# Kernel tuning notes

Measured on AMD Instinct MI355X. Metric: run time of the kernel, lower is better.

## Reference

```python
import jax, jax.numpy as jnp
import numpy as np

HIDDEN = 1024
NUM_HEADS = 8
HEAD_DIM = HIDDEN // NUM_HEADS
ROPE_BASE = 10000.0
RMS_EPS = 1e-6


def _rotate_half(x):
    # interleaved rotate: (x0,x1,x2,x3,...) -> (-x1,x0,-x3,x2,...)
    x1 = x[..., ::2]
    x2 = x[..., 1::2]
    return jnp.stack([-x2, x1], axis=-1).reshape(x.shape)


def _rope_cos_sin(seq_len, rotary_dim, dtype):
    inv_freq = 1.0 / (ROPE_BASE ** (jnp.arange(0, rotary_dim, 2, dtype=jnp.float32) / rotary_dim))
    pos = jnp.arange(seq_len, dtype=jnp.float32)
    freqs = pos[:, None] * inv_freq[None, :]            # [S, rd/2]
    cos = jnp.repeat(jnp.cos(freqs), 2, axis=-1)        # [S, rd]
    sin = jnp.repeat(jnp.sin(freqs), 2, axis=-1)
    return cos.astype(dtype)[None, None], sin.astype(dtype)[None, None]


def setup_inputs() -> dict:
    key = jax.random.key(0)
    k = jax.random.split(key, 8)
    B, S, H = 2, 2048, HIDDEN
    hidden_states = jax.random.normal(k[0], (B, S, H), dtype=jnp.float32)
    attention_mask = jax.random.randint(k[1], (B, S, S), 0, 2) > 0
    rel_ts_bias = jax.random.normal(k[2], (B, S, S), dtype=jnp.float32)
    s1 = 1.0 / np.sqrt(H)
    W_qkvu = jax.random.normal(k[3], (H, H * 6), dtype=jnp.float32) * s1
    W_out = jax.random.normal(k[4], (H * 3, H), dtype=jnp.float32) * (1.0 / np.sqrt(H * 3))
    b_out = jnp.zeros((H,), dtype=jnp.float32)
    rms_weight = jnp.ones((H,), dtype=jnp.float32)
    return {"hidden_states": hidden_states, "attention_mask": attention_mask,
            "rel_ts_bias": rel_ts_bias, "W_qkvu": W_qkvu, "W_out": W_out,
            "b_out": b_out, "rms_weight": rms_weight}


def reference(hidden_states, attention_mask, rel_ts_bias, W_qkvu, W_out, b_out, rms_weight):
    B, S, H = hidden_states.shape
    nh, hd = NUM_HEADS, HEAD_DIM
    fused = jax.nn.silu(hidden_states @ W_qkvu)          # [B,S,6H]
    gated = fused[..., :3 * H]                            # [B,S,3H]
    v = fused[..., 3 * H:4 * H].reshape(B, S, nh, hd).transpose(0, 2, 1, 3)
    q = fused[..., 4 * H:5 * H].reshape(B, S, nh, hd).transpose(0, 2, 1, 3)
    kk = fused[..., 5 * H:].reshape(B, S, nh, hd).transpose(0, 2, 1, 3)

    cos, sin = _rope_cos_sin(S, hd, hidden_states.dtype)  # rotary_dim == head_dim
    q_rope = q * cos + _rotate_half(q) * sin
    k_rope = kk * cos + _rotate_half(kk) * sin

    inv_s = 1.0 / max(S, 1)
    qk = jax.nn.relu(jnp.einsum('bhnd,bhmd->bhnm', q, kk)) * inv_s
    qk_rope = jax.nn.relu(jnp.einsum('bhnd,bhmd->bhnm', q_rope, k_rope)) * inv_s

    mask = attention_mask[:, None]                        # [B,1,S,S]
    qk = jnp.where(mask, qk, 0.0)
    qk_rope = jnp.where(mask, qk_rope, 0.0)
    ts_bias = jnp.where(attention_mask, rel_ts_bias, 0.0)

    ts_out = jnp.einsum('bnm,bhmd->bnhd', ts_bias, v)
    rope_out = jnp.einsum('bhnm,bhmd->bnhd', qk_rope, v)
    plain_out = jnp.einsum('bhnm,bhmd->bnhd', qk, v)

    combined = jnp.concatenate([rope_out, ts_out, plain_out], axis=-1).reshape(B, S, 3 * H)
    out = (combined * gated) @ W_out + b_out
    y = out + hidden_states
    rms = jax.lax.rsqrt(jnp.mean(y * y, axis=-1, keepdims=True) + RMS_EPS)
    return y * rms * rms_weight
```

## Files before the change

### kernel.cpp

```cpp
#include <hip/hip_runtime.h>
#include <math.h>

static constexpr int Bz = 2;
static constexpr int Sq = 2048;
static constexpr int Hh = 1024;
static constexpr int NH = 8;
static constexpr int HD = 128;
static constexpr int H3 = 3072;
static constexpr int H6 = 6144;

typedef unsigned short ushort_t;
typedef float f32x4v __attribute__((ext_vector_type(4)));
typedef short s16x8 __attribute__((ext_vector_type(8)));

static constexpr size_t FUSED_OFF = 0;
static constexpr size_t A2_OFF    = 12582912;
static constexpr size_t HB_OFF    = 18874368;
static constexpr size_t MTB_OFF   = 18874368;
static constexpr size_t WQT_OFF   = 20971520;
static constexpr size_t WOT_OFF   = 24117248;
static constexpr size_t QR_OFF    = 25690112;
static constexpr size_t KR_OFF    = 27787264;
static constexpr size_t VT_OFF    = 29884416;
static constexpr size_t TAB_OFF   = 31981568;
static constexpr size_t FLAG_OFF  = 32243712;
static constexpr size_t TSB_OFF   = 32243716;

__device__ __forceinline__ float silu_(float x) { return x / (1.0f + expf(-x)); }
__device__ __forceinline__ ushort_t f2bf(float x) {
  unsigned int u = __float_as_uint(x);
  u += 0x7fffu + ((u >> 16) & 1u);
  return (ushort_t)(u >> 16);
}
__device__ __forceinline__ float bf2f(ushort_t u) {
  return __uint_as_float(((unsigned int)u) << 16);
}
__device__ __forceinline__ void g2l16(const ushort_t* g, ushort_t* l) {
  __builtin_amdgcn_global_load_lds(
      (const __attribute__((address_space(1))) unsigned int*)g,
      (__attribute__((address_space(3))) unsigned int*)l, 16, 0, 0);
}

__global__ __launch_bounds__(256) void hstu_pre(const unsigned int* __restrict__ m,
                                                int* __restrict__ flag,
                                                float* __restrict__ tab) {
  __shared__ int s_any;
  if (blockIdx.x == 512) {
    if (threadIdx.x == 0) s_any = 0;
    __syncthreads();
    int any = 0;
    for (int i = threadIdx.x; i < 8192; i += 256)
      if (m[i] > 1u) any = 1;
    if (any) s_any = 1;
    __syncthreads();
    if (threadIdx.x == 0) *flag = s_any;
    return;
  }
  int t = blockIdx.x * 256 + threadIdx.x;
  int i = t & 63;
  int s = t >> 6;
  float inv = powf(10000.0f, -(float)i / 64.0f);
  float sn, cs;
  sincosf((float)s * inv, &sn, &cs);
  tab[2 * t + 0] = cs;
  tab[2 * t + 1] = sn;
}

__global__ __launch_bounds__(256) void hstu_msk(const int* __restrict__ mask32,
                                                const unsigned char* __restrict__ mask8,
                                                const int* __restrict__ mflag,
                                                const float* __restrict__ bias,
                                                ushort_t* __restrict__ tsb,
                                                ushort_t* __restrict__ mtb) {
  const size_t base = ((size_t)blockIdx.x * 256 + threadIdx.x) * 8;
  const int m_u8 = *mflag;
  const ushort_t ivs = f2bf(1.0f / 2048.0f);
  int mk[8];
  if (m_u8) {
    uchar4 a = *(const uchar4*)&mask8[base];
    uchar4 b = *(const uchar4*)&mask8[base + 4];
    mk[0] = a.x; mk[1] = a.y; mk[2] = a.z; mk[3] = a.w;
    mk[4] = b.x; mk[5] = b.y; mk[6] = b.z; mk[7] = b.w;
  } else {
    int4 a = *(const int4*)&mask32[base];
    int4 b = *(const int4*)&mask32[base + 4];
    mk[0] = a.x; mk[1] = a.y; mk[2] = a.z; mk[3] = a.w;
    mk[4] = b.x; mk[5] = b.y; mk[6] = b.z; mk[7] = b.w;
  }
  float4 b0 = *(const float4*)&bias[base];
  float4 b1 = *(const float4*)&bias[base + 4];
  float bb[8] = {b0.x, b0.y, b0.z, b0.w, b1.x, b1.y, b1.z, b1.w};
  ushort_t ts[8], mt[8];
#pragma unroll
  for (int i = 0; i < 8; ++i) {
    ts[i] = f2bf(mk[i] ? bb[i] : 0.0f);
    mt[i] = mk[i] ? ivs : (ushort_t)0u;
  }
  *(s16x8*)&tsb[base] = *(s16x8*)ts;
  *(s16x8*)&mtb[base] = *(s16x8*)mt;
}

__global__ __launch_bounds__(256) void hstu_cvt_all(const float* __restrict__ hidden,
                                                    ushort_t* __restrict__ hb,
                                                    const float* __restrict__ Wq,
                                                    ushort_t* __restrict__ wqt,
                                                    const float* __restrict__ Wo,
                                                    ushort_t* __restrict__ wot) {
  __shared__ float tbuf[32][33];
  const int blk = blockIdx.x;
  if (blk < 4096) {
    const int idx = blk * 256 + threadIdx.x;
    float4 v = *(const float4*)&hidden[(size_t)idx * 4];
    ushort4 o;
    o.x = f2bf(v.x); o.y = f2bf(v.y); o.z = f2bf(v.z); o.w = f2bf(v.w);
    *(ushort4*)&hb[(size_t)idx * 4] = o;
    return;
  }
  const float* in;
  ushort_t* out;
  int K, N, n0, k0;
  if (blk < 4096 + 6144) {
    const int j = blk - 4096;
    in = Wq; out = wqt; K = 1024; N = 6144;
    n0 = (j % 192) * 32; k0 = (j / 192) * 32;
  } else {
    const int j = blk - 10240;
    in = Wo; out = wot; K = 3072; N = 1024;
    n0 = (j % 32) * 32; k0 = (j / 32) * 32;
  }
  const int c = threadIdx.x & 31, rr = threadIdx.x >> 5;
#pragma unroll
  for (int p = 0; p < 4; ++p)
    tbuf[rr + p * 8][c] = in[(size_t)(k0 + rr + p * 8) * N + n0 + c];
  __syncthreads();
#pragma unroll
  for (int p = 0; p < 4; ++p)
    out[(size_t)(n0 + rr + p * 8) * K + k0 + c] = f2bf(tbuf[c][rr + p * 8]);
}

__global__ __launch_bounds__(256) void hstu_prep2(const ushort_t* __restrict__ fused,
                                                  const float2* __restrict__ tab,
                                                  ushort_t* __restrict__ qr,
                                                  ushort_t* __restrict__ kr,
                                                  ushort_t* __restrict__ vt) {
  __shared__ ushort_t tbuf[32][36];
  const int blk = blockIdx.x;
  if (blk < 2048) {
    const int idx = blk * 256 + threadIdx.x;
    const int row = idx >> 7;
    const int cg = (idx & 127) * 8;
    const int s = row & (Sq - 1);
    const float2* trow = &tab[(size_t)s * 64 + ((cg & 127) >> 1)];
    float2 t[4];
#pragma unroll
    for (int p = 0; p < 4; ++p) t[p] = trow[p];
    s16x8 q8 = *(const s16x8*)&fused[(size_t)row * H6 + 4 * Hh + cg];
    s16x8 k8 = *(const s16x8*)&fused[(size_t)row * H6 + 5 * Hh + cg];
    ushort_t qo[8], ko[8];
#pragma unroll
    for (int p = 0; p < 4; ++p) {
      float qx = bf2f((ushort_t)q8[2 * p]), qy = bf2f((ushort_t)q8[2 * p + 1]);
      float kx = bf2f((ushort_t)k8[2 * p]), ky = bf2f((ushort_t)k8[2 * p + 1]);
      qo[2 * p] = f2bf(qx * t[p].x - qy * t[p].y);
      qo[2 * p + 1] = f2bf(qy * t[p].x + qx * t[p].y);
      ko[2 * p] = f2bf(kx * t[p].x - ky * t[p].y);
      ko[2 * p + 1] = f2bf(ky * t[p].x + kx * t[p].y);
    }
    *(s16x8*)&qr[(size_t)row * Hh + cg] = *(s16x8*)qo;
    *(s16x8*)&kr[(size_t)row * Hh + cg] = *(s16x8*)ko;
    return;
  }
  const int j = blk - 2048;
  const int m0 = (j & 63) * 32, d0 = ((j >> 6) & 3) * 32, bh = j >> 8;
  const int b = bh >> 3, h = bh & 7;
  const int r = threadIdx.x >> 3, cg = (threadIdx.x & 7) * 4;
  *(ushort4*)&tbuf[r][cg] =
      *(const ushort4*)&fused[(size_t)(b * Sq + m0 + r) * H6 + 3 * Hh + h * HD + d0 + cg];
  __syncthreads();
  ushort4 o;
  o.x = tbuf[cg + 0][r]; o.y = tbuf[cg + 1][r]; o.z = tbuf[cg + 2][r]; o.w = tbuf[cg + 3][r];
  *(ushort4*)&vt[(size_t)(bh * HD + d0 + r) * Sq + m0 + cg] = o;
}

__global__ __launch_bounds__(256) void hstu_gemm_silu(const ushort_t* __restrict__ A,
                                                      const ushort_t* __restrict__ Bt,
                                                      ushort_t* __restrict__ C) {
  constexpr int K = 1024, N = H6;
  __shared__ ushort_t As[128 * 64];
  __shared__ ushort_t Bs[128 * 64];
  const int tid = threadIdx.x, lane = tid & 63, wid = tid >> 6;
  const int lo4 = lane & 15, hi2 = lane >> 4;
  const int wr = wid >> 1, wc = wid & 1;
  const int row0 = blockIdx.y * 128, col0 = blockIdx.x * 128;
  const int srow = lane >> 3, scol = (lane & 7) * 8;
  f32x4v acc[4][4];
#pragma unroll
  for (int i = 0; i < 4; ++i)
#pragma unroll
    for (int j = 0; j < 4; ++j) acc[i][j] = {0.f, 0.f, 0.f, 0.f};

  for (int k0 = 0; k0 < K; k0 += 64) {
    __syncthreads();
#pragma unroll
    for (int i = 0; i < 4; ++i) {
      const int rb = wid * 32 + i * 8;
      g2l16(&A[(size_t)(row0 + rb + srow) * K + k0 + scol], &As[rb * 64]);
      g2l16(&Bt[(size_t)(col0 + rb + srow) * K + k0 + scol], &Bs[rb * 64]);
    }
    __syncthreads();
#pragma unroll
    for (int kc = 0; kc < 2; ++kc) {
      s16x8 af[4], bfr[4];
#pragma unroll
      for (int mi = 0; mi < 4; ++mi)
        af[mi] = *(const s16x8*)&As[(wr * 64 + mi * 16 + lo4) * 64 + kc * 32 + hi2 * 8];
#pragma unroll
      for (int nj = 0; nj < 4; ++nj)
        bfr[nj] = *(const s16x8*)&Bs[(wc * 64 + nj * 16 + lo4) * 64 + kc * 32 + hi2 * 8];
#pragma unroll
      for (int mi = 0; mi < 4; ++mi)
#pragma unroll
        for (int nj = 0; nj < 4; ++nj)
          acc[mi][nj] = __builtin_amdgcn_mfma_f32_16x16x32_bf16(af[mi], bfr[nj], acc[mi][nj], 0, 0, 0);
    }
  }
#pragma unroll
  for (int mi = 0; mi < 4; ++mi)
#pragma unroll
    for (int nj = 0; nj < 4; ++nj)
#pragma unroll
      for (int r = 0; r < 4; ++r) {
        const int row = row0 + wr * 64 + mi * 16 + hi2 * 4 + r;
        const int col = col0 + wc * 64 + nj * 16 + lo4;
        C[(size_t)row * N + col] = f2bf(silu_(acc[mi][nj][r]));
      }
}

__global__ __launch_bounds__(256) void hstu_gemm_out(const ushort_t* __restrict__ A,
                                                     const ushort_t* __restrict__ Bt,
                                                     const float* __restrict__ bout,
                                                     const float* __restrict__ hidden,
                                                     float* __restrict__ C) {
  constexpr int K = H3, N = Hh;
  __shared__ ushort_t As[128 * 64];
  __shared__ ushort_t Bs[64 * 64];
  const int tid = threadIdx.x, lane = tid & 63, wid = tid >> 6;
  const int lo4 = lane & 15, hi2 = lane >> 4;
  const int wr = wid >> 1, wc = wid & 1;
  const int row0 = blockIdx.y * 128, col0 = blockIdx.x * 64;
  const int srow = lane >> 3, scol = (lane & 7) * 8;
  f32x4v acc[4][2];
#pragma unroll
  for (int i = 0; i < 4; ++i)
#pragma unroll
    for (int j = 0; j < 2; ++j) acc[i][j] = {0.f, 0.f, 0.f, 0.f};

  for (int k0 = 0; k0 < K; k0 += 64) {
    __syncthreads();
#pragma unroll
    for (int i = 0; i < 4; ++i) {
      const int rb = wid * 32 + i * 8;
      g2l16(&A[(size_t)(row0 + rb + srow) * K + k0 + scol], &As[rb * 64]);
    }
#pragma unroll
    for (int i = 0; i < 2; ++i) {
      const int rb = wid * 16 + i * 8;
      g2l16(&Bt[(size_t)(col0 + rb + srow) * K + k0 + scol], &Bs[rb * 64]);
    }
    __syncthreads();
#pragma unroll
    for (int kc = 0; kc < 2; ++kc) {
      s16x8 af[4], bfr[2];
#pragma unroll
      for (int mi = 0; mi < 4; ++mi)
        af[mi] = *(const s16x8*)&As[(wr * 64 + mi * 16 + lo4) * 64 + kc * 32 + hi2 * 8];
#pragma unroll
      for (int nj = 0; nj < 2; ++nj)
        bfr[nj] = *(const s16x8*)&Bs[(wc * 32 + nj * 16 + lo4) * 64 + kc * 32 + hi2 * 8];
#pragma unroll
      for (int mi = 0; mi < 4; ++mi)
#pragma unroll
        for (int nj = 0; nj < 2; ++nj)
          acc[mi][nj] = __builtin_amdgcn_mfma_f32_16x16x32_bf16(af[mi], bfr[nj], acc[mi][nj], 0, 0, 0);
    }
  }
#pragma unroll
  for (int mi = 0; mi < 4; ++mi)
#pragma unroll
    for (int nj = 0; nj < 2; ++nj)
#pragma unroll
      for (int r = 0; r < 4; ++r) {
        const int row = row0 + wr * 64 + mi * 16 + hi2 * 4 + r;
        const int col = col0 + wc * 32 + nj * 16 + lo4;
        C[(size_t)row * N + col] = acc[mi][nj][r] + bout[col] + hidden[(size_t)row * N + col];
      }
}

__global__ __launch_bounds__(512, 4) void hstu_attn(const ushort_t* __restrict__ fused,
                                                    const ushort_t* __restrict__ qr,
                                                    const ushort_t* __restrict__ kr,
                                                    const ushort_t* __restrict__ vt,
                                                    const ushort_t* __restrict__ tsb,
                                                    const ushort_t* __restrict__ mtb,
                                                    ushort_t* __restrict__ a2) {
  __shared__ __align__(16) ushort_t Ks[32][136];
  __shared__ __align__(16) ushort_t KRs[32][136];
  __shared__ __align__(16) ushort_t Vt[2][128][40];
  __shared__ __align__(16) ushort_t Pl[2][64][40];
  __shared__ __align__(16) ushort_t Pts[2][64][40];
  __shared__ __align__(16) ushort_t Mt[64][40];

  const int tid = threadIdx.x;
  const int lane = tid & 63;
  const int wid = tid >> 6;
  const int lo4 = lane & 15;
  const int hi2 = lane >> 4;
  const int h = blockIdx.x;
  const int n0 = blockIdx.y * 64;
  const int b = blockIdx.z;
  constexpr int NT = Sq / 32;

  const int krow = tid >> 4, kcol = (tid & 15) * 8;
  const int vdd = tid >> 2, vmg = (tid & 3) * 8;
  const int trow = (tid & 255) >> 2, tmg = (tid & 3) * 8;
  const ushort_t* TM = (wid < 4) ? tsb : mtb;
  const size_t kbase = (size_t)b * Sq * H6 + 5 * Hh + h * HD + kcol;
  const size_t krbase = (size_t)b * Sq * Hh + h * HD + kcol;
  const size_t vbase = (size_t)((b * NH + h) * HD + vdd) * Sq + vmg;
  const size_t tbase = (size_t)(b * Sq + n0 + trow) * Sq + tmg;

  const int t_w = wid >> 2;
  const int rq = wid & 3;
  s16x8 qf[4];
  {
    const int row = tid >> 4;
    const int colg = (tid & 15) * 8;
#pragma unroll
    for (int half = 0; half < 2; ++half) {
      const size_t gr = (size_t)(b * Sq + n0 + half * 32 + row);
      *(s16x8*)&Ks[row][colg] = *(const s16x8*)&fused[gr * H6 + 4 * Hh + h * HD + colg];
      *(s16x8*)&KRs[row][colg] = *(const s16x8*)&qr[gr * Hh + h * HD + colg];
      __syncthreads();
      if ((rq >> 1) == half) {
        const int lrow = (rq & 1) * 16 + lo4;
        const ushort_t(*Qsrc)[136] = t_w ? KRs : Ks;
#pragma unroll
        for (int c = 0; c < 4; ++c)
          qf[c] = *(const s16x8*)&Qsrc[lrow][c * 32 + hi2 * 8];
      }
      __syncthreads();
    }
  }

  const f32x4v zero4 = {0.f, 0.f, 0.f, 0.f};
  f32x4v accO[3][2][2];
#pragma unroll
  for (int t = 0; t < 3; ++t)
#pragma unroll
    for (int rt = 0; rt < 2; ++rt)
#pragma unroll
      for (int ct = 0; ct < 2; ++ct) accO[t][rt][ct] = zero4;

  const int rh2 = wid >> 2;
  const int cq = wid & 3;

  s16x8 kreg, krreg, vreg, tmreg;
#define LOADT(T)                                                            \
  {                                                                         \
    const size_t moff = (size_t)(T) * 32;                                   \
    kreg = *(const s16x8*)&fused[kbase + (moff + krow) * H6];               \
    krreg = *(const s16x8*)&kr[krbase + (moff + krow) * Hh];                \
    vreg = *(const s16x8*)&vt[vbase + moff];                                \
    tmreg = *(const s16x8*)&TM[tbase + moff];                               \
  }
#define WRITET(BUF)                                                         \
  {                                                                         \
    *(s16x8*)&Ks[krow][kcol] = kreg;                                        \
    *(s16x8*)&KRs[krow][kcol] = krreg;                                      \
    *(s16x8*)&Vt[BUF][vdd][vmg] = vreg;                                     \
    if (wid < 4) *(s16x8*)&Pts[BUF][trow][tmg] = tmreg;                     \
    else *(s16x8*)&Mt[trow][tmg] = tmreg;                                   \
  }

  LOADT(0);
  WRITET(0);
  __syncthreads();

  for (int t = 0; t < NT; ++t) {
    const int cur = t & 1;
    if (t + 1 < NT) LOADT(t + 1);
    {
      const ushort_t(*Kmat)[136] = t_w ? KRs : Ks;
      const int n = rq * 16 + lo4;
#pragma unroll
      for (int mt2 = 0; mt2 < 2; ++mt2) {
        f32x4v a = zero4;
#pragma unroll
        for (int c = 0; c < 4; ++c) {
          s16x8 kf = *(const s16x8*)&Kmat[mt2 * 16 + lo4][c * 32 + hi2 * 8];
          a = __builtin_amdgcn_mfma_f32_16x16x32_bf16(kf, qf[c], a, 0, 0, 0);
        }
        const int mb = mt2 * 16 + hi2 * 4;
        ushort4 mt4 = *(const ushort4*)&Mt[n][mb];
        ushort4 po;
        po.x = f2bf(fmaxf(a[0], 0.f) * bf2f(mt4.x));
        po.y = f2bf(fmaxf(a[1], 0.f) * bf2f(mt4.y));
        po.z = f2bf(fmaxf(a[2], 0.f) * bf2f(mt4.z));
        po.w = f2bf(fmaxf(a[3], 0.f) * bf2f(mt4.w));
        *(ushort4*)&Pl[t_w][n][mb] = po;
      }
    }
    __syncthreads();
    {
      s16x8 af[3][2];
#pragma unroll
      for (int rt = 0; rt < 2; ++rt) {
        af[0][rt] = *(const s16x8*)&Pl[0][rh2 * 32 + rt * 16 + lo4][hi2 * 8];
        af[1][rt] = *(const s16x8*)&Pl[1][rh2 * 32 + rt * 16 + lo4][hi2 * 8];
        af[2][rt] = *(const s16x8*)&Pts[cur][rh2 * 32 + rt * 16 + lo4][hi2 * 8];
      }
      s16x8 bfv[2];
#pragma unroll
      for (int ct = 0; ct < 2; ++ct)
        bfv[ct] = *(const s16x8*)&Vt[cur][cq * 32 + ct * 16 + lo4][hi2 * 8];
      if (t + 1 < NT) WRITET(cur ^ 1);
#pragma unroll
      for (int ty = 0; ty < 3; ++ty)
#pragma unroll
        for (int rt = 0; rt < 2; ++rt)
#pragma unroll
          for (int ct = 0; ct < 2; ++ct)
            accO[ty][rt][ct] =
                __builtin_amdgcn_mfma_f32_16x16x32_bf16(af[ty][rt], bfv[ct], accO[ty][rt][ct], 0, 0, 0);
    }
    __syncthreads();
  }
#undef LOADT
#undef WRITET

  const int toff[3] = {256, 0, 128};
#pragma unroll
  for (int ty = 0; ty < 3; ++ty)
#pragma unroll
    for (int rt = 0; rt < 2; ++rt)
#pragma unroll
      for (int ct = 0; ct < 2; ++ct)
#pragma unroll
        for (int r = 0; r < 4; ++r) {
          const int n = n0 + rh2 * 32 + rt * 16 + hi2 * 4 + r;
          const int dd = cq * 32 + ct * 16 + lo4;
          const int col3 = h * 384 + toff[ty] + dd;
          const float g = bf2f(fused[(size_t)(b * Sq + n) * H6 + col3]);
          a2[(size_t)(b * Sq + n) * H3 + col3] = f2bf(accO[ty][rt][ct][r] * g);
        }
}

__global__ __launch_bounds__(256) void hstu_rms(float* __restrict__ y,
                                                const float* __restrict__ w) {
  __shared__ float red[4];
  const int row = blockIdx.x;
  const int tid = threadIdx.x;
  float4 v = *(float4*)&y[(size_t)row * Hh + tid * 4];
  float ss = v.x * v.x + v.y * v.y + v.z * v.z + v.w * v.w;
#pragma unroll
  for (int o = 32; o > 0; o >>= 1) ss += __shfl_down(ss, o);
  if ((tid & 63) == 0) red[tid >> 6] = ss;
  __syncthreads();
  const float tot = red[0] + red[1] + red[2] + red[3];
  const float r = 1.0f / sqrtf(tot / (float)Hh + 1e-6f);
  float4 wv = *(const float4*)&w[tid * 4];
  v.x *= r * wv.x;
  v.y *= r * wv.y;
  v.z *= r * wv.z;
  v.w *= r * wv.w;
  *(float4*)&y[(size_t)row * Hh + tid * 4] = v;
}

extern "C" void kernel_launch(void* const* d_in, const int* in_sizes, int n_in,
                              void* d_out, int out_size, void* d_ws, size_t ws_size,
                              hipStream_t stream) {
  const float* hidden = (const float*)d_in[0];
  const void* mask = d_in[1];
  const float* bias = (const float*)d_in[2];
  const float* Wqkvu = (const float*)d_in[3];
  const float* Wout = (const float*)d_in[4];
  const float* bout = (const float*)d_in[5];
  const float* rmsw = (const float*)d_in[6];
  float* out = (float*)d_out;
  float* ws = (float*)d_ws;

  ushort_t* fused = (ushort_t*)(ws + FUSED_OFF);
  ushort_t* a2 = (ushort_t*)(ws + A2_OFF);
  ushort_t* hb = (ushort_t*)(ws + HB_OFF);
  ushort_t* mtbp = (ushort_t*)(ws + MTB_OFF);
  ushort_t* wqt = (ushort_t*)(ws + WQT_OFF);
  ushort_t* wot = (ushort_t*)(ws + WOT_OFF);
  ushort_t* qrb = (ushort_t*)(ws + QR_OFF);
  ushort_t* krb = (ushort_t*)(ws + KR_OFF);
  ushort_t* vtb = (ushort_t*)(ws + VT_OFF);
  float* tab = ws + TAB_OFF;
  int* mflag = (int*)(ws + FLAG_OFF);
  ushort_t* tsbp = (ushort_t*)(ws + TSB_OFF);

  hstu_pre<<<513, 256, 0, stream>>>((const unsigned int*)mask, mflag, tab);
  hstu_cvt_all<<<13312, 256, 0, stream>>>(hidden, hb, Wqkvu, wqt, Wout, wot);
  hstu_gemm_silu<<<dim3(H6 / 128, (Bz * Sq) / 128), 256, 0, stream>>>(hb, wqt, fused);
  hstu_msk<<<(Bz * Sq * Sq / 8) / 256, 256, 0, stream>>>(
      (const int*)mask, (const unsigned char*)mask, mflag, bias, tsbp, mtbp);
  hstu_prep2<<<6144, 256, 0, stream>>>(fused, (const float2*)tab, qrb, krb, vtb);
  hstu_attn<<<dim3(NH, Sq / 64, Bz), 512, 0, stream>>>(fused, qrb, krb, vtb, tsbp, mtbp, a2);
  hstu_gemm_out<<<dim3(Hh / 64, (Bz * Sq) / 128), 256, 0, stream>>>(a2, wot, bout, hidden, out);
  hstu_rms<<<Bz * Sq, 256, 0, stream>>>(out, rmsw);
}
```

Before: 327.6 us.

## Pack attention mask into bits and fuse mask prep into QKV GEMM launch

Replaces the bf16 per-element mask tensor with a 1-bit-per-element mask, cutting the bytes written by preprocessing and read by attention. The mask/bias preprocessing is merged into the QKV GEMM launch as extra blocks so the two independent jobs can overlap. The attention kernel drops LDS double-buffering of the V/ts tiles and uses single buffers plus an extra barrier per step, which frees shared memory but serializes the tile writes with compute.

```diff
diff --git a/kernel.cpp b/kernel.cpp
--- a/kernel.cpp
+++ b/kernel.cpp
@@ -16,7 +16,6 @@
 static constexpr size_t FUSED_OFF = 0;
 static constexpr size_t A2_OFF    = 12582912;
 static constexpr size_t HB_OFF    = 18874368;
-static constexpr size_t MTB_OFF   = 18874368;
 static constexpr size_t WQT_OFF   = 20971520;
 static constexpr size_t WOT_OFF   = 24117248;
 static constexpr size_t QR_OFF    = 25690112;
@@ -25,6 +24,7 @@
 static constexpr size_t TAB_OFF   = 31981568;
 static constexpr size_t FLAG_OFF  = 32243712;
 static constexpr size_t TSB_OFF   = 32243716;
+static constexpr size_t MBITS_OFF = 36438020;
 
 __device__ __forceinline__ float silu_(float x) { return x / (1.0f + expf(-x)); }
 __device__ __forceinline__ ushort_t f2bf(float x) {
@@ -64,40 +64,6 @@
   sincosf((float)s * inv, &sn, &cs);
   tab[2 * t + 0] = cs;
   tab[2 * t + 1] = sn;
-}
-
-__global__ __launch_bounds__(256) void hstu_msk(const int* __restrict__ mask32,
-                                                const unsigned char* __restrict__ mask8,
-                                                const int* __restrict__ mflag,
-                                                const float* __restrict__ bias,
-                                                ushort_t* __restrict__ tsb,
-                                                ushort_t* __restrict__ mtb) {
-  const size_t base = ((size_t)blockIdx.x * 256 + threadIdx.x) * 8;
-  const int m_u8 = *mflag;
-  const ushort_t ivs = f2bf(1.0f / 2048.0f);
-  int mk[8];
-  if (m_u8) {
-    uchar4 a = *(const uchar4*)&mask8[base];
-    uchar4 b = *(const uchar4*)&mask8[base + 4];
-    mk[0] = a.x; mk[1] = a.y; mk[2] = a.z; mk[3] = a.w;
-    mk[4] = b.x; mk[5] = b.y; mk[6] = b.z; mk[7] = b.w;
-  } else {
-    int4 a = *(const int4*)&mask32[base];
-    int4 b = *(const int4*)&mask32[base + 4];
-    mk[0] = a.x; mk[1] = a.y; mk[2] = a.z; mk[3] = a.w;
-    mk[4] = b.x; mk[5] = b.y; mk[6] = b.z; mk[7] = b.w;
-  }
-  float4 b0 = *(const float4*)&bias[base];
-  float4 b1 = *(const float4*)&bias[base + 4];
-  float bb[8] = {b0.x, b0.y, b0.z, b0.w, b1.x, b1.y, b1.z, b1.w};
-  ushort_t ts[8], mt[8];
-#pragma unroll
-  for (int i = 0; i < 8; ++i) {
-    ts[i] = f2bf(mk[i] ? bb[i] : 0.0f);
-    mt[i] = mk[i] ? ivs : (ushort_t)0u;
-  }
-  *(s16x8*)&tsb[base] = *(s16x8*)ts;
-  *(s16x8*)&mtb[base] = *(s16x8*)mt;
 }
 
 __global__ __launch_bounds__(256) void hstu_cvt_all(const float* __restrict__ hidden,
@@ -138,6 +104,95 @@
     out[(size_t)(n0 + rr + p * 8) * K + k0 + c] = f2bf(tbuf[c][rr + p * 8]);
 }
 
+__global__ __launch_bounds__(256) void hstu_gemm_silu_msk(
+    const ushort_t* __restrict__ A, const ushort_t* __restrict__ Bt,
+    ushort_t* __restrict__ C, const int* __restrict__ mask32,
+    const unsigned char* __restrict__ mask8, const int* __restrict__ mflag,
+    const float* __restrict__ bias, ushort_t* __restrict__ tsb,
+    unsigned char* __restrict__ mbits) {
+  __shared__ ushort_t As[128 * 64];
+  __shared__ ushort_t Bs[128 * 64];
+  const int blk = blockIdx.x;
+  const int tid = threadIdx.x;
+  if (blk >= 1536) {
+    const size_t gt = (size_t)(blk - 1536) * 256 + tid;
+    const size_t base = gt * 8;
+    const int m_u8 = *mflag;
+    int mk[8];
+    if (m_u8) {
+      uchar4 a = *(const uchar4*)&mask8[base];
+      uchar4 b = *(const uchar4*)&mask8[base + 4];
+      mk[0] = a.x; mk[1] = a.y; mk[2] = a.z; mk[3] = a.w;
+      mk[4] = b.x; mk[5] = b.y; mk[6] = b.z; mk[7] = b.w;
+    } else {
+      int4 a = *(const int4*)&mask32[base];
+      int4 b = *(const int4*)&mask32[base + 4];
+      mk[0] = a.x; mk[1] = a.y; mk[2] = a.z; mk[3] = a.w;
+      mk[4] = b.x; mk[5] = b.y; mk[6] = b.z; mk[7] = b.w;
+    }
+    float4 b0 = *(const float4*)&bias[base];
+    float4 b1 = *(const float4*)&bias[base + 4];
+    float bb[8] = {b0.x, b0.y, b0.z, b0.w, b1.x, b1.y, b1.z, b1.w};
+    ushort_t ts[8];
+    unsigned int byte = 0;
+#pragma unroll
+    for (int i = 0; i < 8; ++i) {
+      ts[i] = f2bf(mk[i] ? bb[i] : 0.0f);
+      byte |= (mk[i] ? 1u : 0u) << i;
+    }
+    *(s16x8*)&tsb[base] = *(s16x8*)ts;
+    mbits[gt] = (unsigned char)byte;
+    return;
+  }
+  constexpr int K = 1024, N = H6;
+  const int lane = tid & 63, wid = tid >> 6;
+  const int lo4 = lane & 15, hi2 = lane >> 4;
+  const int wr = wid >> 1, wc = wid & 1;
+  const int row0 = (blk / 48) * 128, col0 = (blk % 48) * 128;
+  const int srow = lane >> 3, scol = (lane & 7) * 8;
+  f32x4v acc[4][4];
+#pragma unroll
+  for (int i = 0; i < 4; ++i)
+#pragma unroll
+    for (int j = 0; j < 4; ++j) acc[i][j] = {0.f, 0.f, 0.f, 0.f};
+
+  for (int k0 = 0; k0 < K; k0 += 64) {
+    __syncthreads();
+#pragma unroll
+    for (int i = 0; i < 4; ++i) {
+      const int rb = wid * 32 + i * 8;
+      g2l16(&A[(size_t)(row0 + rb + srow) * K + k0 + scol], &As[rb * 64]);
+      g2l16(&Bt[(size_t)(col0 + rb + srow) * K + k0 + scol], &Bs[rb * 64]);
+    }
+    __syncthreads();
+#pragma unroll
+    for (int kc = 0; kc < 2; ++kc) {
+      s16x8 af[4], bfr[4];
+#pragma unroll
+      for (int mi = 0; mi < 4; ++mi)
+        af[mi] = *(const s16x8*)&As[(wr * 64 + mi * 16 + lo4) * 64 + kc * 32 + hi2 * 8];
+#pragma unroll
+      for (int nj = 0; nj < 4; ++nj)
+        bfr[nj] = *(const s16x8*)&Bs[(wc * 64 + nj * 16 + lo4) * 64 + kc * 32 + hi2 * 8];
+#pragma unroll
+      for (int mi = 0; mi < 4; ++mi)
+#pragma unroll
+        for (int nj = 0; nj < 4; ++nj)
+          acc[mi][nj] = __builtin_amdgcn_mfma_f32_16x16x32_bf16(af[mi], bfr[nj], acc[mi][nj], 0, 0, 0);
+    }
+  }
+#pragma unroll
+  for (int mi = 0; mi < 4; ++mi)
+#pragma unroll
+    for (int nj = 0; nj < 4; ++nj)
+#pragma unroll
+      for (int r = 0; r < 4; ++r) {
+        const int row = row0 + wr * 64 + mi * 16 + hi2 * 4 + r;
+        const int col = col0 + wc * 64 + nj * 16 + lo4;
+        C[(size_t)row * N + col] = f2bf(silu_(acc[mi][nj][r]));
+      }
+}
+
 __global__ __launch_bounds__(256) void hstu_prep2(const ushort_t* __restrict__ fused,
                                                   const float2* __restrict__ tab,
                                                   ushort_t* __restrict__ qr,
@@ -182,60 +237,6 @@
   *(ushort4*)&vt[(size_t)(bh * HD + d0 + r) * Sq + m0 + cg] = o;
 }
 
-__global__ __launch_bounds__(256) void hstu_gemm_silu(const ushort_t* __restrict__ A,
-                                                      const ushort_t* __restrict__ Bt,
-                                                      ushort_t* __restrict__ C) {
-  constexpr int K = 1024, N = H6;
-  __shared__ ushort_t As[128 * 64];
-  __shared__ ushort_t Bs[128 * 64];
-  const int tid = threadIdx.x, lane = tid & 63, wid = tid >> 6;
-  const int lo4 = lane & 15, hi2 = lane >> 4;
-  const int wr = wid >> 1, wc = wid & 1;
-  const int row0 = blockIdx.y * 128, col0 = blockIdx.x * 128;
-  const int srow = lane >> 3, scol = (lane & 7) * 8;
-  f32x4v acc[4][4];
-#pragma unroll
-  for (int i = 0; i < 4; ++i)
-#pragma unroll
-    for (int j = 0; j < 4; ++j) acc[i][j] = {0.f, 0.f, 0.f, 0.f};
-
-  for (int k0 = 0; k0 < K; k0 += 64) {
-    __syncthreads();
-#pragma unroll
-    for (int i = 0; i < 4; ++i) {
-      const int rb = wid * 32 + i * 8;
-      g2l16(&A[(size_t)(row0 + rb + srow) * K + k0 + scol], &As[rb * 64]);
-      g2l16(&Bt[(size_t)(col0 + rb + srow) * K + k0 + scol], &Bs[rb * 64]);
-    }
-    __syncthreads();
-#pragma unroll
-    for (int kc = 0; kc < 2; ++kc) {
-      s16x8 af[4], bfr[4];
-#pragma unroll
-      for (int mi = 0; mi < 4; ++mi)
-        af[mi] = *(const s16x8*)&As[(wr * 64 + mi * 16 + lo4) * 64 + kc * 32 + hi2 * 8];
-#pragma unroll
-      for (int nj = 0; nj < 4; ++nj)
-        bfr[nj] = *(const s16x8*)&Bs[(wc * 64 + nj * 16 + lo4) * 64 + kc * 32 + hi2 * 8];
-#pragma unroll
-      for (int mi = 0; mi < 4; ++mi)
-#pragma unroll
-        for (int nj = 0; nj < 4; ++nj)
-          acc[mi][nj] = __builtin_amdgcn_mfma_f32_16x16x32_bf16(af[mi], bfr[nj], acc[mi][nj], 0, 0, 0);
-    }
-  }
-#pragma unroll
-  for (int mi = 0; mi < 4; ++mi)
-#pragma unroll
-    for (int nj = 0; nj < 4; ++nj)
-#pragma unroll
-      for (int r = 0; r < 4; ++r) {
-        const int row = row0 + wr * 64 + mi * 16 + hi2 * 4 + r;
-        const int col = col0 + wc * 64 + nj * 16 + lo4;
-        C[(size_t)row * N + col] = f2bf(silu_(acc[mi][nj][r]));
-      }
-}
-
 __global__ __launch_bounds__(256) void hstu_gemm_out(const ushort_t* __restrict__ A,
                                                      const ushort_t* __restrict__ Bt,
                                                      const float* __restrict__ bout,
@@ -301,14 +302,13 @@
                                                     const ushort_t* __restrict__ kr,
                                                     const ushort_t* __restrict__ vt,
                                                     const ushort_t* __restrict__ tsb,
-                                                    const ushort_t* __restrict__ mtb,
+                                                    const unsigned int* __restrict__ mbits32,
                                                     ushort_t* __restrict__ a2) {
   __shared__ __align__(16) ushort_t Ks[32][136];
   __shared__ __align__(16) ushort_t KRs[32][136];
-  __shared__ __align__(16) ushort_t Vt[2][128][40];
-  __shared__ __align__(16) ushort_t Pl[2][64][40];
-  __shared__ __align__(16) ushort_t Pts[2][64][40];
-  __shared__ __align__(16) ushort_t Mt[64][40];
+  __shared__ __align__(16) ushort_t Vt[128][40];
+  __shared__ __align__(16) ushort_t Pl[3][64][40];
+  __shared__ unsigned int Mt32[64];
 
   const int tid = threadIdx.x;
   const int lane = tid & 63;
@@ -318,16 +318,17 @@
   const int h = blockIdx.x;
   const int n0 = blockIdx.y * 64;
   const int b = blockIdx.z;
+  const float ivs = 1.0f / 2048.0f;
   constexpr int NT = Sq / 32;
 
   const int krow = tid >> 4, kcol = (tid & 15) * 8;
   const int vdd = tid >> 2, vmg = (tid & 3) * 8;
   const int trow = (tid & 255) >> 2, tmg = (tid & 3) * 8;
-  const ushort_t* TM = (wid < 4) ? tsb : mtb;
   const size_t kbase = (size_t)b * Sq * H6 + 5 * Hh + h * HD + kcol;
   const size_t krbase = (size_t)b * Sq * Hh + h * HD + kcol;
   const size_t vbase = (size_t)((b * NH + h) * HD + vdd) * Sq + vmg;
   const size_t tbase = (size_t)(b * Sq + n0 + trow) * Sq + tmg;
+  const size_t mbase = (size_t)(b * Sq + n0 + lane) * 64;
 
   const int t_w = wid >> 2;
   const int rq = wid & 3;
@@ -364,34 +365,36 @@
   const int rh2 = wid >> 2;
   const int cq = wid & 3;
 
-  s16x8 kreg, krreg, vreg, tmreg;
+  s16x8 kreg, krreg, vreg, tsreg;
+  unsigned int mreg;
 #define LOADT(T)                                                            \
   {                                                                         \
     const size_t moff = (size_t)(T) * 32;                                   \
     kreg = *(const s16x8*)&fused[kbase + (moff + krow) * H6];               \
     krreg = *(const s16x8*)&kr[krbase + (moff + krow) * Hh];                \
     vreg = *(const s16x8*)&vt[vbase + moff];                                \
-    tmreg = *(const s16x8*)&TM[tbase + moff];                               \
-  }
-#define WRITET(BUF)                                                         \
+    if (wid < 4) tsreg = *(const s16x8*)&tsb[tbase + moff];                 \
+    else if (wid == 4) mreg = mbits32[mbase + (T)];                         \
+  }
+#define WRITET()                                                            \
   {                                                                         \
     *(s16x8*)&Ks[krow][kcol] = kreg;                                        \
     *(s16x8*)&KRs[krow][kcol] = krreg;                                      \
-    *(s16x8*)&Vt[BUF][vdd][vmg] = vreg;                                     \
-    if (wid < 4) *(s16x8*)&Pts[BUF][trow][tmg] = tmreg;                     \
-    else *(s16x8*)&Mt[trow][tmg] = tmreg;                                   \
+    *(s16x8*)&Vt[vdd][vmg] = vreg;                                          \
+    if (wid < 4) *(s16x8*)&Pl[2][trow][tmg] = tsreg;                        \
+    else if (wid == 4) Mt32[lane] = mreg;                                   \
   }
 
   LOADT(0);
-  WRITET(0);
+  WRITET();
   __syncthreads();
 
   for (int t = 0; t < NT; ++t) {
-    const int cur = t & 1;
     if (t + 1 < NT) LOADT(t + 1);
     {
       const ushort_t(*Kmat)[136] = t_w ? KRs : Ks;
       const int n = rq * 16 + lo4;
+      const unsigned int bits = Mt32[n];
 #pragma unroll
       for (int mt2 = 0; mt2 < 2; ++mt2) {
         f32x4v a = zero4;
@@ -401,12 +404,11 @@
           a = __builtin_amdgcn_mfma_f32_16x16x32_bf16(kf, qf[c], a, 0, 0, 0);
         }
         const int mb = mt2 * 16 + hi2 * 4;
-        ushort4 mt4 = *(const ushort4*)&Mt[n][mb];
         ushort4 po;
-        po.x = f2bf(fmaxf(a[0], 0.f) * bf2f(mt4.x));
-        po.y = f2bf(fmaxf(a[1], 0.f) * bf2f(mt4.y));
-        po.z = f2bf(fmaxf(a[2], 0.f) * bf2f(mt4.z));
-        po.w = f2bf(fmaxf(a[3], 0.f) * bf2f(mt4.w));
+        po.x = ((bits >> (mb + 0)) & 1u) ? f2bf(fmaxf(a[0], 0.f) * ivs) : (ushort_t)0;
+        po.y = ((bits >> (mb + 1)) & 1u) ? f2bf(fmaxf(a[1], 0.f) * ivs) : (ushort_t)0;
+        po.z = ((bits >> (mb + 2)) & 1u) ? f2bf(fmaxf(a[2], 0.f) * ivs) : (ushort_t)0;
+        po.w = ((bits >> (mb + 3)) & 1u) ? f2bf(fmaxf(a[3], 0.f) * ivs) : (ushort_t)0;
         *(ushort4*)&Pl[t_w][n][mb] = po;
       }
     }
@@ -414,16 +416,14 @@
     {
       s16x8 af[3][2];
 #pragma unroll
-      for (int rt = 0; rt < 2; ++rt) {
-        af[0][rt] = *(const s16x8*)&Pl[0][rh2 * 32 + rt * 16 + lo4][hi2 * 8];
-        af[1][rt] = *(const s16x8*)&Pl[1][rh2 * 32 + rt * 16 + lo4][hi2 * 8];
-        af[2][rt] = *(const s16x8*)&Pts[cur][rh2 * 32 + rt * 16 + lo4][hi2 * 8];
-      }
+      for (int ty = 0; ty < 3; ++ty)
+#pragma unroll
+        for (int rt = 0; rt < 2; ++rt)
+          af[ty][rt] = *(const s16x8*)&Pl[ty][rh2 * 32 + rt * 16 + lo4][hi2 * 8];
       s16x8 bfv[2];
 #pragma unroll
       for (int ct = 0; ct < 2; ++ct)
-        bfv[ct] = *(const s16x8*)&Vt[cur][cq * 32 + ct * 16 + lo4][hi2 * 8];
-      if (t + 1 < NT) WRITET(cur ^ 1);
+        bfv[ct] = *(const s16x8*)&Vt[cq * 32 + ct * 16 + lo4][hi2 * 8];
 #pragma unroll
       for (int ty = 0; ty < 3; ++ty)
 #pragma unroll
@@ -433,6 +433,8 @@
             accO[ty][rt][ct] =
                 __builtin_amdgcn_mfma_f32_16x16x32_bf16(af[ty][rt], bfv[ct], accO[ty][rt][ct], 0, 0, 0);
     }
+    __syncthreads();
+    if (t + 1 < NT) WRITET();
     __syncthreads();
   }
 #undef LOADT
@@ -492,7 +494,6 @@
   ushort_t* fused = (ushort_t*)(ws + FUSED_OFF);
   ushort_t* a2 = (ushort_t*)(ws + A2_OFF);
   ushort_t* hb = (ushort_t*)(ws + HB_OFF);
-  ushort_t* mtbp = (ushort_t*)(ws + MTB_OFF);
   ushort_t* wqt = (ushort_t*)(ws + WQT_OFF);
   ushort_t* wot = (ushort_t*)(ws + WOT_OFF);
   ushort_t* qrb = (ushort_t*)(ws + QR_OFF);
@@ -501,14 +502,15 @@
   float* tab = ws + TAB_OFF;
   int* mflag = (int*)(ws + FLAG_OFF);
   ushort_t* tsbp = (ushort_t*)(ws + TSB_OFF);
+  unsigned char* mbits = (unsigned char*)(ws + MBITS_OFF);
 
   hstu_pre<<<513, 256, 0, stream>>>((const unsigned int*)mask, mflag, tab);
   hstu_cvt_all<<<13312, 256, 0, stream>>>(hidden, hb, Wqkvu, wqt, Wout, wot);
-  hstu_gemm_silu<<<dim3(H6 / 128, (Bz * Sq) / 128), 256, 0, stream>>>(hb, wqt, fused);
-  hstu_msk<<<(Bz * Sq * Sq / 8) / 256, 256, 0, stream>>>(
-      (const int*)mask, (const unsigned char*)mask, mflag, bias, tsbp, mtbp);
+  hstu_gemm_silu_msk<<<1536 + 4096, 256, 0, stream>>>(
+      hb, wqt, fused, (const int*)mask, (const unsigned char*)mask, mflag, bias, tsbp, mbits);
   hstu_prep2<<<6144, 256, 0, stream>>>(fused, (const float2*)tab, qrb, krb, vtb);
-  hstu_attn<<<dim3(NH, Sq / 64, Bz), 512, 0, stream>>>(fused, qrb, krb, vtb, tsbp, mtbp, a2);
+  hstu_attn<<<dim3(NH, Sq / 64, Bz), 512, 0, stream>>>(
+      fused, qrb, krb, vtb, tsbp, (const unsigned int*)mbits, a2);
   hstu_gemm_out<<<dim3(Hh / 64, (Bz * Sq) / 128), 256, 0, stream>>>(a2, wot, bout, hidden, out);
   hstu_rms<<<Bz * Sq, 256, 0, stream>>>(out, rmsw);
 }
```

After: 310.8 us. 1.05x faster.
